# Kernel tuning notes

Measured on AMD Instinct MI355X. Metric: run time of the kernel, lower is better.

## Reference

```python
import jax, jax.numpy as jnp
import numpy as np

EPS = 1e-5  # torch InstanceNorm2d / LayerNorm default eps


def setup_inputs() -> dict:
    key = jax.random.key(0)
    k1, k2, k3 = jax.random.split(key, 3)
    B, C, H, W_ = 8, 256, 128, 128
    x = jax.random.normal(k1, (B, C, H, W_), dtype=jnp.float32)
    params = jax.random.normal(k2, (B, 2 * C), dtype=jnp.float32)
    # Conv2d(dim*2, dim, 1) weight, squeezed to [C_out, C_in]
    W = jax.random.normal(k3, (C, 2 * C), dtype=jnp.float32) * (1.0 / np.sqrt(2 * C))
    return {"x": x, "params": params, "W": W}


def reference(x, params, W):
    # x: [B, C, H, W]; params: [B, 2C]; W: [C, 2C]
    C = x.shape[1]
    # InstanceNorm2d (no affine): normalize over spatial dims per (b, c), biased var
    in_mean = jnp.mean(x, axis=(2, 3), keepdims=True)
    in_var = jnp.var(x, axis=(2, 3), keepdims=True)
    IN = (x - in_mean) * jax.lax.rsqrt(in_var + EPS)
    # LayerNorm over (C, H, W) per sample, biased var
    ln_mean = jnp.mean(x, axis=(1, 2, 3), keepdims=True)
    ln_var = jnp.var(x, axis=(1, 2, 3), keepdims=True)
    LN = (x - ln_mean) * jax.lax.rsqrt(ln_var + EPS)
    LIN = jnp.concatenate((IN, LN), axis=1)  # [B, 2C, H, W]
    # 1x1 conv == channel contraction
    c = jnp.einsum('bihw,oi->bohw', LIN, W)  # [B, C, H, W]
    gamma = params[:, :C][:, :, None, None]
    beta = params[:, C:][:, :, None, None]
    return gamma * c + beta
```

## Files before the change

kernel.cpp:

```cpp
#include <hip/hip_runtime.h>
#include <stdint.h>

#define HW_  16384
#define CH   256
#define NB   8
#define EPSV 1e-5f

typedef float f32x4 __attribute__((ext_vector_type(4)));
typedef short s16x8 __attribute__((ext_vector_type(8)));

__device__ __forceinline__ unsigned short f2bf(float f) {
    union { float f; uint32_t u; } v; v.f = f;
    uint32_t r = (v.u + 0x7FFFu + ((v.u >> 16) & 1u)) >> 16;
    return (unsigned short)r;
}

__global__ __launch_bounds__(256) void stats_kernel(const float* __restrict__ x,
                                                    float* __restrict__ sums,
                                                    float* __restrict__ sumsq) {
    const int bc  = blockIdx.x;
    const int tid = threadIdx.x;
    const float4* p = reinterpret_cast<const float4*>(x + (size_t)bc * HW_);
    float s = 0.f, q = 0.f;
#pragma unroll 4
    for (int i = tid; i < HW_ / 4; i += 256) {
        float4 v = p[i];
        s += v.x + v.y + v.z + v.w;
        q += v.x * v.x + v.y * v.y + v.z * v.z + v.w * v.w;
    }
    __shared__ float rs[256], rq[256];
    rs[tid] = s; rq[tid] = q;
    __syncthreads();
    for (int off = 128; off > 0; off >>= 1) {
        if (tid < off) { rs[tid] += rs[tid + off]; rq[tid] += rq[tid + off]; }
        __syncthreads();
    }
    if (tid == 0) { sums[bc] = rs[0]; sumsq[bc] = rq[0]; }
}

__global__ __launch_bounds__(256) void prep_kernel(const float* __restrict__ sums,
                                                   const float* __restrict__ sumsq,
                                                   const float* __restrict__ params,
                                                   const float* __restrict__ W,
                                                   unsigned short* __restrict__ Ap,
                                                   float* __restrict__ Dp) {
    const int b   = blockIdx.x;
    const int tid = threadIdx.x;
    __shared__ float mu[CH], ri[CH], rs[CH], rq[CH];
    float s = sums[b * CH + tid];
    float q = sumsq[b * CH + tid];
    float m = s * (1.0f / HW_);
    float v = q * (1.0f / HW_) - m * m;
    mu[tid] = m;
    ri[tid] = rsqrtf(v + EPSV);
    rs[tid] = s; rq[tid] = q;
    __syncthreads();
    for (int off = 128; off > 0; off >>= 1) {
        if (tid < off) { rs[tid] += rs[tid + off]; rq[tid] += rq[tid + off]; }
        __syncthreads();
    }
    const float invN = 1.0f / ((float)CH * (float)HW_);
    const float mln  = rs[0] * invN;
    const float vln  = rq[0] * invN - mln * mln;
    const float rln  = rsqrtf(vln + EPSV);

    const int o = tid;
    const float gamma = params[b * 2 * CH + o];
    const float beta  = params[b * 2 * CH + CH + o];
    const float4* w1p = reinterpret_cast<const float4*>(W + (size_t)o * 2 * CH);
    const float4* w2p = reinterpret_cast<const float4*>(W + (size_t)o * 2 * CH + CH);
    unsigned short* aprow = Ap + ((size_t)(b * CH + o)) * CH;
    float t1 = 0.f, t2 = 0.f;
    for (int c4 = 0; c4 < CH / 4; ++c4) {
        float4 w1 = w1p[c4];
        float4 w2 = w2p[c4];
        float w1a[4] = {w1.x, w1.y, w1.z, w1.w};
        float w2a[4] = {w2.x, w2.y, w2.z, w2.w};
        const int c = c4 * 4;
        ushort4 pk;
        unsigned short* pka = (unsigned short*)&pk;
#pragma unroll
        for (int j = 0; j < 4; ++j) {
            float ric = ri[c + j];
            float a   = gamma * (w1a[j] * ric + w2a[j] * rln);
            pka[j] = f2bf(a);
            t1 += w1a[j] * ric * mu[c + j];
            t2 += w2a[j];
        }
        *reinterpret_cast<ushort4*>(aprow + c) = pk;
    }
    const float d = -(t1 + rln * mln * t2);
    Dp[b * CH + o] = gamma * d + beta;
}

__global__ __launch_bounds__(512) void gemm_kernel(const float* __restrict__ x,
                                                   const unsigned short* __restrict__ Ap,
                                                   const float* __restrict__ Dp,
                                                   float* __restrict__ out) {
    __shared__ unsigned short As[4 * 256 * 8];
    __shared__ unsigned short Xs[4 * 128 * 8];

    const int b   = blockIdx.y;
    const int n0  = blockIdx.x * 128;
    const int t   = threadIdx.x;
    const int w   = t >> 6;
    const int l   = t & 63;
    const int wm  = w >> 1;
    const int wn  = w & 1;
    const int lhi = l >> 4;
    const int llo = l & 15;

    f32x4 acc[4][4];
    const float* dpb = Dp + b * CH;
#pragma unroll
    for (int fm = 0; fm < 4; ++fm) {
        const int mb = wm * 64 + fm * 16 + lhi * 4;
        f32x4 d;
        d.x = dpb[mb + 0]; d.y = dpb[mb + 1]; d.z = dpb[mb + 2]; d.w = dpb[mb + 3];
#pragma unroll
        for (int fn = 0; fn < 4; ++fn) acc[fm][fn] = d;
    }

    const size_t xbase = (size_t)b * CH * HW_ + n0;
    const unsigned short* apb = Ap + (size_t)b * CH * CH;
    uint32_t* Xs32 = reinterpret_cast<uint32_t*>(Xs);

    const int am  = t & 255;
    const int ag0 = t >> 8;
    const int kp  = t >> 5;
    const int nq  = t & 31;
    const int xg  = kp >> 2;
    const int xh  = kp & 3;

    for (int kb = 0; kb < 8; ++kb) {
        const int k0 = kb * 32;
        s16x8 areg0 = *reinterpret_cast<const s16x8*>(apb + (size_t)am * CH + k0 + (ag0 + 0) * 8);
        s16x8 areg1 = *reinterpret_cast<const s16x8*>(apb + (size_t)am * CH + k0 + (ag0 + 2) * 8);
        f32x4 xa = *reinterpret_cast<const f32x4*>(x + xbase + (size_t)(k0 + 2 * kp + 0) * HW_ + nq * 4);
        f32x4 xb = *reinterpret_cast<const f32x4*>(x + xbase + (size_t)(k0 + 2 * kp + 1) * HW_ + nq * 4);

        __syncthreads();

        *reinterpret_cast<s16x8*>(&As[(ag0 + 0) * 2048 + am * 8]) = areg0;
        *reinterpret_cast<s16x8*>(&As[(ag0 + 2) * 2048 + am * 8]) = areg1;
#pragma unroll
        for (int j = 0; j < 4; ++j) {
            uint32_t pk = (uint32_t)f2bf(xa[j]) | ((uint32_t)f2bf(xb[j]) << 16);
            Xs32[xg * 512 + (nq * 4 + j) * 4 + xh] = pk;
        }

        __syncthreads();

        s16x8 af[4], bfr[4];
#pragma unroll
        for (int fm = 0; fm < 4; ++fm)
            af[fm] = *reinterpret_cast<const s16x8*>(&As[lhi * 2048 + (wm * 64 + fm * 16 + llo) * 8]);
#pragma unroll
        for (int fn = 0; fn < 4; ++fn)
            bfr[fn] = *reinterpret_cast<const s16x8*>(&Xs[lhi * 1024 + (wn * 64 + fn * 16 + llo) * 8]);
#pragma unroll
        for (int fm = 0; fm < 4; ++fm)
#pragma unroll
            for (int fn = 0; fn < 4; ++fn)
                acc[fm][fn] = __builtin_amdgcn_mfma_f32_16x16x32_bf16(af[fm], bfr[fn], acc[fm][fn], 0, 0, 0);
    }

#pragma unroll
    for (int fm = 0; fm < 4; ++fm) {
        const int m = wm * 64 + fm * 16 + lhi * 4;
        float* obase = out + (size_t)(b * CH + m) * HW_ + n0 + wn * 64 + llo;
#pragma unroll
        for (int fn = 0; fn < 4; ++fn) {
#pragma unroll
            for (int r = 0; r < 4; ++r)
                obase[(size_t)r * HW_ + fn * 16] = acc[fm][fn][r];
        }
    }
}

extern "C" void kernel_launch(void* const* d_in, const int* in_sizes, int n_in,
                              void* d_out, int out_size, void* d_ws, size_t ws_size,
                              hipStream_t stream) {
    const float* x      = (const float*)d_in[0];
    const float* params = (const float*)d_in[1];
    const float* W      = (const float*)d_in[2];
    float* out = (float*)d_out;
    float* ws  = (float*)d_ws;

    float* sums  = ws;
    float* sumsq = ws + 2048;
    float* Dp    = ws + 4096;
    unsigned short* Ap = (unsigned short*)(ws + 6144);

    hipLaunchKernelGGL(stats_kernel, dim3(NB * CH), dim3(256), 0, stream, x, sums, sumsq);
    hipLaunchKernelGGL(prep_kernel,  dim3(NB),      dim3(256), 0, stream, sums, sumsq, params, W, Ap, Dp);
    hipLaunchKernelGGL(gemm_kernel,  dim3(HW_ / 128, NB), dim3(512), 0, stream, x, Ap, Dp, out);
}
```

Baseline: 116.2 us.

## Prefetch next K-tile into registers and swizzle X shared layout in GEMM

```diff
diff --git a/kernel.cpp b/kernel.cpp
--- a/kernel.cpp
+++ b/kernel.cpp
@@ -93,10 +93,10 @@
     Dp[b * CH + o] = gamma * d + beta;
 }
 
-__global__ __launch_bounds__(512) void gemm_kernel(const float* __restrict__ x,
-                                                   const unsigned short* __restrict__ Ap,
-                                                   const float* __restrict__ Dp,
-                                                   float* __restrict__ out) {
+__global__ __launch_bounds__(512, 4) void gemm_kernel(const float* __restrict__ x,
+                                                      const unsigned short* __restrict__ Ap,
+                                                      const float* __restrict__ Dp,
+                                                      float* __restrict__ out) {
     __shared__ unsigned short As[4 * 256 * 8];
     __shared__ unsigned short Xs[4 * 128 * 8];
 
@@ -114,9 +114,7 @@
     const float* dpb = Dp + b * CH;
 #pragma unroll
     for (int fm = 0; fm < 4; ++fm) {
-        const int mb = wm * 64 + fm * 16 + lhi * 4;
-        f32x4 d;
-        d.x = dpb[mb + 0]; d.y = dpb[mb + 1]; d.z = dpb[mb + 2]; d.w = dpb[mb + 3];
+        f32x4 d = *reinterpret_cast<const f32x4*>(dpb + wm * 64 + fm * 16 + lhi * 4);
 #pragma unroll
         for (int fn = 0; fn < 4; ++fn) acc[fm][fn] = d;
     }
@@ -132,37 +130,51 @@
     const int xg  = kp >> 2;
     const int xh  = kp & 3;
 
+    int npr[4];
+#pragma unroll
+    for (int fn = 0; fn < 4; ++fn) {
+        const int nr = wn * 64 + fn * 16 + llo;
+        npr[fn] = nr ^ ((nr >> 3) & 7);
+    }
+
+    s16x8 areg0 = *reinterpret_cast<const s16x8*>(apb + (size_t)am * CH + (ag0 + 0) * 8);
+    s16x8 areg1 = *reinterpret_cast<const s16x8*>(apb + (size_t)am * CH + (ag0 + 2) * 8);
+    f32x4 xa = *reinterpret_cast<const f32x4*>(x + xbase + (size_t)(2 * kp + 0) * HW_ + nq * 4);
+    f32x4 xb = *reinterpret_cast<const f32x4*>(x + xbase + (size_t)(2 * kp + 1) * HW_ + nq * 4);
+
+#pragma unroll
     for (int kb = 0; kb < 8; ++kb) {
-        const int k0 = kb * 32;
-        s16x8 areg0 = *reinterpret_cast<const s16x8*>(apb + (size_t)am * CH + k0 + (ag0 + 0) * 8);
-        s16x8 areg1 = *reinterpret_cast<const s16x8*>(apb + (size_t)am * CH + k0 + (ag0 + 2) * 8);
-        f32x4 xa = *reinterpret_cast<const f32x4*>(x + xbase + (size_t)(k0 + 2 * kp + 0) * HW_ + nq * 4);
-        f32x4 xb = *reinterpret_cast<const f32x4*>(x + xbase + (size_t)(k0 + 2 * kp + 1) * HW_ + nq * 4);
-
         __syncthreads();
 
         *reinterpret_cast<s16x8*>(&As[(ag0 + 0) * 2048 + am * 8]) = areg0;
         *reinterpret_cast<s16x8*>(&As[(ag0 + 2) * 2048 + am * 8]) = areg1;
 #pragma unroll
         for (int j = 0; j < 4; ++j) {
+            const int n  = nq * 4 + j;
+            const int np = n ^ ((n >> 3) & 7);
             uint32_t pk = (uint32_t)f2bf(xa[j]) | ((uint32_t)f2bf(xb[j]) << 16);
-            Xs32[xg * 512 + (nq * 4 + j) * 4 + xh] = pk;
-        }
-
-        __syncthreads();
-
-        s16x8 af[4], bfr[4];
+            Xs32[xg * 512 + np * 4 + xh] = pk;
+        }
+
+        __syncthreads();
+
+        const int k0n = (kb < 7 ? kb + 1 : 7) * 32;
+        areg0 = *reinterpret_cast<const s16x8*>(apb + (size_t)am * CH + k0n + (ag0 + 0) * 8);
+        areg1 = *reinterpret_cast<const s16x8*>(apb + (size_t)am * CH + k0n + (ag0 + 2) * 8);
+        xa = *reinterpret_cast<const f32x4*>(x + xbase + (size_t)(k0n + 2 * kp + 0) * HW_ + nq * 4);
+        xb = *reinterpret_cast<const f32x4*>(x + xbase + (size_t)(k0n + 2 * kp + 1) * HW_ + nq * 4);
+
+        s16x8 af[4];
 #pragma unroll
         for (int fm = 0; fm < 4; ++fm)
             af[fm] = *reinterpret_cast<const s16x8*>(&As[lhi * 2048 + (wm * 64 + fm * 16 + llo) * 8]);
 #pragma unroll
-        for (int fn = 0; fn < 4; ++fn)
-            bfr[fn] = *reinterpret_cast<const s16x8*>(&Xs[lhi * 1024 + (wn * 64 + fn * 16 + llo) * 8]);
-#pragma unroll
-        for (int fm = 0; fm < 4; ++fm)
-#pragma unroll
-            for (int fn = 0; fn < 4; ++fn)
-                acc[fm][fn] = __builtin_amdgcn_mfma_f32_16x16x32_bf16(af[fm], bfr[fn], acc[fm][fn], 0, 0, 0);
+        for (int fn = 0; fn < 4; ++fn) {
+            s16x8 bfr = *reinterpret_cast<const s16x8*>(&Xs[lhi * 1024 + npr[fn] * 8]);
+#pragma unroll
+            for (int fm = 0; fm < 4; ++fm)
+                acc[fm][fn] = __builtin_amdgcn_mfma_f32_16x16x32_bf16(af[fm], bfr, acc[fm][fn], 0, 0, 0);
+        }
     }
 
 #pragma unroll
```

Result: slower. 132.3 us (+13.8%).
